# Kernel optimization log

Measured on AMD Instinct MI355X. Metric: run time of the kernel, lower is better.

Reference implementation:

```python
import jax, jax.numpy as jnp
import numpy as np

N_DISEASE = 50000
N_GENE = 50000
D = 64
N_EDGES = 2000000

def setup_inputs() -> dict:
    key = jax.random.key(0)
    k1, k2, k3, k4, k5, k6 = jax.random.split(key, 6)
    return {
        "x_disease": jax.random.normal(k1, (N_DISEASE, D), dtype=jnp.float32),
        "h_disease": jax.random.normal(k2, (N_DISEASE, D), dtype=jnp.float32),
        "x_gene": jax.random.normal(k3, (N_GENE, D), dtype=jnp.float32),
        "h_gene": jax.random.normal(k4, (N_GENE, D), dtype=jnp.float32),
        "src": jax.random.randint(k5, (N_EDGES,), 0, N_DISEASE, dtype=jnp.int32),
        "dst": jax.random.randint(k6, (N_EDGES,), 0, N_GENE, dtype=jnp.int32),
    }

def reference(x_disease, h_disease, x_gene, h_gene, src, dst):
    # Concat raw and learned features per node type: [N, 2D]
    f_d = jnp.concatenate([x_disease, h_disease], axis=1)
    f_g = jnp.concatenate([x_gene, h_gene], axis=1)
    # Per-node L2 norms: [N, 1]
    n_d = jnp.linalg.norm(f_d, axis=1, keepdims=True)
    n_g = jnp.linalg.norm(f_g, axis=1, keepdims=True)
    # u_dot_v on features: per-edge gather + dot -> [E, 1]
    dot = jnp.sum(f_d[src] * f_g[dst], axis=1, keepdims=True)
    # u_dot_v on norms (1-dim features): product of norms -> [E, 1]
    mou = n_d[src] * n_g[dst]
    return dot / mou
```

## Files before the change

### kernel.cpp

```cpp
#include <hip/hip_runtime.h>


#define FD 64

__device__ __forceinline__ int q8pack(float v0, float v1, float v2, float v3, float inv) {
    float a0 = fminf(fmaxf(v0 * inv, -127.f), 127.f);
    float a1 = fminf(fmaxf(v1 * inv, -127.f), 127.f);
    float a2 = fminf(fmaxf(v2 * inv, -127.f), 127.f);
    float a3 = fminf(fmaxf(v3 * inv, -127.f), 127.f);
    int q0 = ((int)rintf(a0)) & 0xff;
    int q1 = ((int)rintf(a1)) & 0xff;
    int q2 = ((int)rintf(a2)) & 0xff;
    int q3 = ((int)rintf(a3)) & 0xff;
    return q0 | (q1 << 8) | (q2 << 16) | (q3 << 24);
}

__global__ void pack_kernel(const float4* __restrict__ xd, const float4* __restrict__ hd,
                            const float4* __restrict__ xg, const float4* __restrict__ hg,
                            int2* __restrict__ fd, int2* __restrict__ fg,
                            float* __restrict__ sd, float* __restrict__ sg,
                            int n_d, int n_g)
{
    int tid  = (int)(blockIdx.x * blockDim.x + threadIdx.x);
    int node = tid >> 4;
    int lane = threadIdx.x & 15;
    int total = n_d + n_g;
    if (node >= total) return;

    const float4* x; const float4* h; int2* o; float* s; int n;
    if (node < n_d) { x = xd; h = hd; o = fd; s = sd; n = node; }
    else            { x = xg; h = hg; o = fg; s = sg; n = node - n_d; }

    float4 a = x[(size_t)n * 16 + lane];
    float4 b = h[(size_t)n * 16 + lane];

    float ss = a.x*a.x + a.y*a.y + a.z*a.z + a.w*a.w
             + b.x*b.x + b.y*b.y + b.z*b.z + b.w*b.w;
    #pragma unroll
    for (int m = 8; m >= 1; m >>= 1) ss += __shfl_xor(ss, m);
    float r = rsqrtf(ss);

    a.x *= r; a.y *= r; a.z *= r; a.w *= r;
    b.x *= r; b.y *= r; b.z *= r; b.w *= r;

    float mx = fmaxf(fmaxf(fmaxf(fabsf(a.x), fabsf(a.y)), fmaxf(fabsf(a.z), fabsf(a.w))),
                     fmaxf(fmaxf(fabsf(b.x), fabsf(b.y)), fmaxf(fabsf(b.z), fabsf(b.w))));
    #pragma unroll
    for (int m = 8; m >= 1; m >>= 1) mx = fmaxf(mx, __shfl_xor(mx, m));

    float inv = 127.0f / mx;

    int2 w;
    w.x = q8pack(a.x, a.y, a.z, a.w, inv);
    w.y = q8pack(b.x, b.y, b.z, b.w, inv);
    o[(size_t)n * 16 + lane] = w;

    if (lane == 0) s[n] = mx * (1.0f / 127.0f);
}

__device__ __forceinline__ int dot4(int a, int b, int c) {
    return __builtin_amdgcn_sdot4(a, b, c, false);
}

__global__ void edge_kernel(const int4* __restrict__ fd, const int4* __restrict__ fg,
                            const float* __restrict__ sd, const float* __restrict__ sg,
                            const int* __restrict__ src, const int* __restrict__ dst,
                            float* __restrict__ out, int n_edges)
{
    int tid  = (int)(blockIdx.x * blockDim.x + threadIdx.x);
    int lane = threadIdx.x & 7;
    int e    = tid >> 3;
    if (e >= n_edges) return;

    int s = src[e];
    int d = dst[e];

    int4 a = fd[(size_t)s * 8 + lane];
    int4 b = fg[(size_t)d * 8 + lane];

    int acc = dot4(a.x, b.x, dot4(a.y, b.y, dot4(a.z, b.z, dot4(a.w, b.w, 0))));

    acc += __shfl_xor(acc, 4);
    acc += __shfl_xor(acc, 2);
    acc += __shfl_xor(acc, 1);

    if (lane == 0) out[e] = (float)acc * sd[s] * sg[d];
}

extern "C" void kernel_launch(void* const* d_in, const int* in_sizes, int n_in,
                              void* d_out, int out_size, void* d_ws, size_t ws_size,
                              hipStream_t stream) {
    const float* xd = (const float*)d_in[0];
    const float* hd = (const float*)d_in[1];
    const float* xg = (const float*)d_in[2];
    const float* hg = (const float*)d_in[3];
    const int*  src = (const int*)d_in[4];
    const int*  dst = (const int*)d_in[5];

    int n_d     = in_sizes[0] / FD;
    int n_g     = in_sizes[2] / FD;
    int n_edges = in_sizes[4];

    char* ws = (char*)d_ws;
    int2*  fd = (int2*)ws;                       ws += (size_t)n_d * 128;
    int2*  fg = (int2*)ws;                       ws += (size_t)n_g * 128;
    float* sd = (float*)ws;                      ws += (size_t)n_d * sizeof(float);
    float* sg = (float*)ws;
    float* out = (float*)d_out;

    int total_nodes = n_d + n_g;
    int nb1 = (total_nodes * 16 + 255) / 256;
    pack_kernel<<<nb1, 256, 0, stream>>>((const float4*)xd, (const float4*)hd,
                                         (const float4*)xg, (const float4*)hg,
                                         fd, fg, sd, sg, n_d, n_g);

    int nb2 = (int)(((long long)n_edges * 8 + 255) / 256);
    edge_kernel<<<nb2, 256, 0, stream>>>((const int4*)fd, (const int4*)fg,
                                         sd, sg, src, dst, out, n_edges);
}
```

Measured before the change: 167.2 us.

## Sort edges by source via counting sort to reuse source feature rows

After: 492.1 us. 2.94x slower.

```diff
diff --git a/kernel.cpp b/kernel.cpp
--- a/kernel.cpp
+++ b/kernel.cpp
@@ -58,8 +58,84 @@
     if (lane == 0) s[n] = mx * (1.0f / 127.0f);
 }
 
+__global__ void hist_kernel(const int* __restrict__ src, int* __restrict__ cur, int n_edges)
+{
+    int i = (int)(blockIdx.x * blockDim.x + threadIdx.x);
+    if (i < n_edges) atomicAdd(&cur[src[i]], 1);
+}
+
+__global__ void scan_kernel(int* __restrict__ cur, int nbins)
+{
+    __shared__ int psum[1024];
+    int t = threadIdx.x;
+    int chunk = (nbins + 1023) / 1024;
+    int lo = t * chunk;
+    int hi = min(lo + chunk, nbins);
+    int s = 0;
+    for (int i = lo; i < hi; ++i) s += cur[i];
+    psum[t] = s;
+    __syncthreads();
+    if (t == 0) {
+        int acc = 0;
+        for (int i = 0; i < 1024; ++i) { int v = psum[i]; psum[i] = acc; acc += v; }
+    }
+    __syncthreads();
+    int acc = psum[t];
+    for (int i = lo; i < hi; ++i) {
+        int v = cur[i];
+        cur[i] = acc;
+        acc += v;
+    }
+}
+
+__global__ void scatter_kernel(const int* __restrict__ src, const int* __restrict__ dst,
+                               int* __restrict__ cur, int2* __restrict__ sorted, int n_edges)
+{
+    int i = (int)(blockIdx.x * blockDim.x + threadIdx.x);
+    if (i >= n_edges) return;
+    int s = src[i];
+    int d = dst[i];
+    int p = atomicAdd(&cur[s], 1);
+    sorted[p] = make_int2((s << 16) | d, i);
+}
+
 __device__ __forceinline__ int dot4(int a, int b, int c) {
     return __builtin_amdgcn_sdot4(a, b, c, false);
+}
+
+#define CHUNK 32
+
+__global__ void edge_sorted_kernel(const int4* __restrict__ fd, const int4* __restrict__ fg,
+                                   const float* __restrict__ sd, const float* __restrict__ sg,
+                                   const int2* __restrict__ sorted,
+                                   float* __restrict__ out, int n_edges)
+{
+    int tid  = (int)(blockIdx.x * blockDim.x + threadIdx.x);
+    int lane = threadIdx.x & 7;
+    int g    = tid >> 3;
+    int base = g * CHUNK;
+    if (base >= n_edges) return;
+    int lim = min(CHUNK, n_edges - base);
+
+    int s_prev = -1;
+    int4 a = make_int4(0, 0, 0, 0);
+
+    #pragma unroll 4
+    for (int i = 0; i < lim; ++i) {
+        int2 t = sorted[base + i];
+        int s = (int)(((unsigned)t.x) >> 16);
+        int d = t.x & 0xffff;
+        if (s != s_prev) {
+            a = fd[(size_t)s * 8 + lane];
+            s_prev = s;
+        }
+        int4 b = fg[(size_t)d * 8 + lane];
+        int acc = dot4(a.x, b.x, dot4(a.y, b.y, dot4(a.z, b.z, dot4(a.w, b.w, 0))));
+        acc += __shfl_xor(acc, 4);
+        acc += __shfl_xor(acc, 2);
+        acc += __shfl_xor(acc, 1);
+        if (lane == 0) out[t.y] = (float)acc * sd[s] * sg[d];
+    }
 }
 
 __global__ void edge_kernel(const int4* __restrict__ fd, const int4* __restrict__ fg,
@@ -71,19 +147,14 @@
     int lane = threadIdx.x & 7;
     int e    = tid >> 3;
     if (e >= n_edges) return;
-
     int s = src[e];
     int d = dst[e];
-
     int4 a = fd[(size_t)s * 8 + lane];
     int4 b = fg[(size_t)d * 8 + lane];
-
     int acc = dot4(a.x, b.x, dot4(a.y, b.y, dot4(a.z, b.z, dot4(a.w, b.w, 0))));
-
     acc += __shfl_xor(acc, 4);
     acc += __shfl_xor(acc, 2);
     acc += __shfl_xor(acc, 1);
-
     if (lane == 0) out[e] = (float)acc * sd[s] * sg[d];
 }
 
@@ -102,10 +173,12 @@
     int n_edges = in_sizes[4];
 
     char* ws = (char*)d_ws;
-    int2*  fd = (int2*)ws;                       ws += (size_t)n_d * 128;
-    int2*  fg = (int2*)ws;                       ws += (size_t)n_g * 128;
-    float* sd = (float*)ws;                      ws += (size_t)n_d * sizeof(float);
-    float* sg = (float*)ws;
+    int2*  fd  = (int2*)ws;   ws += (size_t)n_d * 128;
+    int2*  fg  = (int2*)ws;   ws += (size_t)n_g * 128;
+    float* sd  = (float*)ws;  ws += (size_t)n_d * sizeof(float);
+    float* sg  = (float*)ws;  ws += (size_t)n_g * sizeof(float);
+    int*   cur = (int*)ws;    ws += (size_t)n_d * sizeof(int);
+    int2*  sorted = (int2*)ws;
     float* out = (float*)d_out;
 
     int total_nodes = n_d + n_g;
@@ -114,7 +187,21 @@
                                          (const float4*)xg, (const float4*)hg,
                                          fd, fg, sd, sg, n_d, n_g);
 
-    int nb2 = (int)(((long long)n_edges * 8 + 255) / 256);
-    edge_kernel<<<nb2, 256, 0, stream>>>((const int4*)fd, (const int4*)fg,
-                                         sd, sg, src, dst, out, n_edges);
-}
+    if (n_d < 65536 && n_g < 65536) {
+        hipMemsetAsync(cur, 0, (size_t)n_d * sizeof(int), stream);
+
+        int nbe = (n_edges + 255) / 256;
+        hist_kernel<<<nbe, 256, 0, stream>>>(src, cur, n_edges);
+        scan_kernel<<<1, 1024, 0, stream>>>(cur, n_d);
+        scatter_kernel<<<nbe, 256, 0, stream>>>(src, dst, cur, sorted, n_edges);
+
+        long long groups = ((long long)n_edges + CHUNK - 1) / CHUNK;
+        int nb4 = (int)((groups * 8 + 255) / 256);
+        edge_sorted_kernel<<<nb4, 256, 0, stream>>>((const int4*)fd, (const int4*)fg,
+                                                    sd, sg, sorted, out, n_edges);
+    } else {
+        int nb2 = (int)(((long long)n_edges * 8 + 255) / 256);
+        edge_kernel<<<nb2, 256, 0, stream>>>((const int4*)fd, (const int4*)fg,
+                                             sd, sg, src, dst, out, n_edges);
+    }
+}
```
